# Optimization experiments

Measured on AMD Instinct MI355X. Metric: run time of the kernel, lower is better.

The kernel has to match this reference:

```python
import jax, jax.numpy as jnp
import numpy as np

D_MODEL = 256
D_HEAD = 64
N_HEAD = 8


def setup_inputs() -> dict:
    key = jax.random.key(0)
    ks = jax.random.split(key, 8)
    b, h, w = 32, 64, 64
    dk = D_HEAD * N_HEAD
    s = 1.0 / np.sqrt(D_MODEL)
    x = jax.random.normal(ks[0], (b, D_MODEL, h, w), dtype=jnp.float32)
    query = jax.random.normal(ks[1], (b, D_MODEL), dtype=jnp.float32)
    Wkv = jax.random.uniform(ks[2], (2 * dk, D_MODEL), jnp.float32, -s, s)
    bkv = jax.random.uniform(ks[3], (2 * dk,), jnp.float32, -s, s)
    Wq = jax.random.uniform(ks[4], (dk, D_MODEL), jnp.float32, -s, s)
    bq = jax.random.uniform(ks[5], (dk,), jnp.float32, -s, s)
    sf = 1.0 / np.sqrt(dk)
    Wfc = jax.random.uniform(ks[6], (D_MODEL, dk), jnp.float32, -sf, sf)
    bfc = jax.random.uniform(ks[7], (D_MODEL,), jnp.float32, -sf, sf)
    return {"x": x, "query": query, "Wkv": Wkv, "bkv": bkv, "Wq": Wq, "bq": bq, "Wfc": Wfc, "bfc": bfc}


def reference(x, query, Wkv, bkv, Wq, bq, Wfc, bfc):
    b, c, h, w = x.shape
    t = h * w
    scale = 1.0 / np.sqrt(D_HEAD).astype(np.float32)
    # 1x1 conv == per-pixel linear: (b, 2*n*d, t)
    kv = jnp.einsum('bchw,oc->bohw', x, Wkv).reshape(b, 2 * N_HEAD, D_HEAD, t)
    kv = kv + bkv.reshape(1, 2 * N_HEAD, D_HEAD, 1)
    k, v = kv[:, :N_HEAD], kv[:, N_HEAD:]  # each (b, n, d, t)
    q = (query @ Wq.T + bq).reshape(b, N_HEAD, D_HEAD)
    logits = jnp.einsum('bnd,bndj->bnj', q, k) * scale
    attn = jax.nn.softmax(logits, axis=2)
    out = jnp.einsum('bnj,bndj->bnd', attn, v).reshape(b, N_HEAD * D_HEAD)
    return jax.nn.relu(out @ Wfc.T + bfc)
```

## Files before the change

### kernel.cpp

```cpp
#include <hip/hip_runtime.h>
#include <hip/hip_bf16.h>

#define B_     32
#define C_     256
#define T_     4096
#define NH_    8
#define DH_    64

__global__ __launch_bounds__(256) void k_prep(
    const float* __restrict__ query, const float* __restrict__ Wkv,
    const float* __restrict__ bkv, const float* __restrict__ Wq,
    const float* __restrict__ bq, float* __restrict__ qWt,
    float* __restrict__ qb) {
  const int n = blockIdx.x;
  const int b = blockIdx.y;
  const int t = threadIdx.x;
  __shared__ float qrow_s[C_];
  __shared__ float psum[4 * 64];
  __shared__ float qsh[64];
  __shared__ float pb_s[64];

  qrow_s[t] = query[(size_t)b * C_ + t];
  __syncthreads();

  {
    const int d = t & 63, ch = t >> 6;
    const float* wrow = Wq + (size_t)(n * DH_ + d) * C_ + ch * 64;
    const float* qr = qrow_s + ch * 64;
    float s = 0.f;
    #pragma unroll
    for (int c = 0; c < 64; c += 4) {
      float4 w = *(const float4*)(wrow + c);
      s += w.x * qr[c] + w.y * qr[c + 1] + w.z * qr[c + 2] + w.w * qr[c + 3];
    }
    psum[ch * 64 + d] = s;
  }
  __syncthreads();
  if (t < 64)
    qsh[t] = bq[n * DH_ + t] + psum[t] + psum[64 + t] + psum[128 + t] + psum[192 + t];
  __syncthreads();

  const float scale = 0.125f;
  {
    const float* wk = Wkv + (size_t)(n * DH_) * C_ + t;
    float acc = 0.f;
    #pragma unroll 8
    for (int dd = 0; dd < DH_; ++dd) acc += qsh[dd] * wk[(size_t)dd * C_];
    qWt[((size_t)b * C_ + t) * NH_ + n] = acc * scale;
  }
  if (t < 64) pb_s[t] = qsh[t] * bkv[n * DH_ + t];
  __syncthreads();
  if (t == 0) {
    float s = 0.f;
    #pragma unroll 8
    for (int dd = 0; dd < 64; ++dd) s += pb_s[dd];
    qb[b * NH_ + n] = s * scale;
  }
}

__global__ __launch_bounds__(256, 4) void k_logits(
    const float* __restrict__ x, const float* __restrict__ qWt,
    const float* __restrict__ qbv, float* __restrict__ lgraw,
    float* __restrict__ stats) {
  const int jt = blockIdx.x;
  const int b  = blockIdx.y;
  const int t  = threadIdx.x;
  const int tj = t & 63;
  const int th = t >> 6;
  __shared__ float qws[C_ * NH_];
  __shared__ float red[4][64][17];

  {
    const float* src = qWt + (size_t)b * (C_ * NH_);
    *(float4*)&qws[t * 4] = *(const float4*)(src + t * 4);
    *(float4*)&qws[1024 + t * 4] = *(const float4*)(src + 1024 + t * 4);
  }
  __syncthreads();

  const int j = jt * 128 + tj * 2;
  const float* xb = x + ((size_t)b * C_ + th * 64) * T_ + j;

  float acc0[NH_], acc1[NH_];
  #pragma unroll
  for (int n = 0; n < NH_; ++n) {
    const float init = (th == 0) ? qbv[b * NH_ + n] : 0.f;
    acc0[n] = init; acc1[n] = init;
  }

  for (int c0 = 0; c0 < 64; c0 += 8) {
    float2 xv[8];
    #pragma unroll
    for (int cc = 0; cc < 8; ++cc)
      xv[cc] = *(const float2*)(xb + (size_t)(c0 + cc) * T_);
    #pragma unroll
    for (int cc = 0; cc < 8; ++cc) {
      const float4 w0 = *(const float4*)(qws + (th * 64 + c0 + cc) * 8);
      const float4 w1 = *(const float4*)(qws + (th * 64 + c0 + cc) * 8 + 4);
      acc0[0] += w0.x * xv[cc].x; acc1[0] += w0.x * xv[cc].y;
      acc0[1] += w0.y * xv[cc].x; acc1[1] += w0.y * xv[cc].y;
      acc0[2] += w0.z * xv[cc].x; acc1[2] += w0.z * xv[cc].y;
      acc0[3] += w0.w * xv[cc].x; acc1[3] += w0.w * xv[cc].y;
      acc0[4] += w1.x * xv[cc].x; acc1[4] += w1.x * xv[cc].y;
      acc0[5] += w1.y * xv[cc].x; acc1[5] += w1.y * xv[cc].y;
      acc0[6] += w1.z * xv[cc].x; acc1[6] += w1.z * xv[cc].y;
      acc0[7] += w1.w * xv[cc].x; acc1[7] += w1.w * xv[cc].y;
    }
  }

  if (th != 0) {
    float* r = &red[th][tj][0];
    #pragma unroll
    for (int n = 0; n < NH_; ++n) { r[n] = acc0[n]; r[8 + n] = acc1[n]; }
  }
  __syncthreads();
  if (th == 0) {
    #pragma unroll
    for (int q = 1; q < 4; ++q) {
      const float* r = &red[q][tj][0];
      #pragma unroll
      for (int n = 0; n < NH_; ++n) { acc0[n] += r[n]; acc1[n] += r[8 + n]; }
    }
    float* lg = lgraw + ((size_t)b * NH_) * T_ + j;
    #pragma unroll
    for (int n = 0; n < NH_; ++n) {
      float2 o; o.x = acc0[n]; o.y = acc1[n];
      *(float2*)(lg + (size_t)n * T_) = o;
    }
    float Mv[NH_], Sv[NH_];
    #pragma unroll
    for (int n = 0; n < NH_; ++n) {
      float mv = fmaxf(acc0[n], acc1[n]);
      #pragma unroll
      for (int o = 32; o >= 1; o >>= 1) mv = fmaxf(mv, __shfl_xor(mv, o));
      Mv[n] = mv;
    }
    #pragma unroll
    for (int n = 0; n < NH_; ++n) {
      float sv = expf(acc0[n] - Mv[n]) + expf(acc1[n] - Mv[n]);
      #pragma unroll
      for (int o = 32; o >= 1; o >>= 1) sv += __shfl_xor(sv, o);
      Sv[n] = sv;
    }
    if (tj == 0) {
      #pragma unroll
      for (int n = 0; n < NH_; ++n) {
        float2 o; o.x = Mv[n]; o.y = Sv[n];
        *(float2*)(stats + ((size_t)(b * NH_ + n) * 32 + jt) * 2) = o;
      }
    }
  }
}

#define BJ_  128
#define BJS_ 32
#define XPITCH_ 33
__global__ __launch_bounds__(256, 4) void k_xattn(
    const float* __restrict__ x, const float* __restrict__ lgraw,
    const float* __restrict__ stats, float* __restrict__ part) {
  const int jt = blockIdx.x;
  const int b  = blockIdx.y;
  const int j0 = jt * BJ_;
  const int t  = threadIdx.x;
  __shared__ float xs[C_ * XPITCH_];
  __shared__ float a_lds[NH_][BJS_];
  __shared__ float Msh[NH_];
  __shared__ float Sish[NH_];

  if (t < NH_) {
    const float* st = stats + (size_t)(b * NH_ + t) * 64;
    float M = -3.4e38f;
    #pragma unroll
    for (int k = 0; k < 32; ++k) M = fmaxf(M, st[k * 2]);
    float S = 0.f;
    #pragma unroll
    for (int k = 0; k < 32; ++k) S += st[k * 2 + 1] * expf(st[k * 2] - M);
    Msh[t] = M; Sish[t] = 1.0f / S;
  }

  const float* xb  = x + (size_t)b * C_ * T_;
  const float* lgb = lgraw + (size_t)b * NH_ * T_ + j0;

  float acc[NH_];
  #pragma unroll
  for (int n = 0; n < NH_; ++n) acc[n] = 0.f;

  const int cr = t >> 3;
  const int jc = (t & 7) * 4;
  const int an = t >> 5;
  const int aj = t & 31;

  for (int sIt = 0; sIt < BJ_ / BJS_; ++sIt) {
    const int js = sIt * BJS_;
    __syncthreads();
    #pragma unroll
    for (int p = 0; p < 8; ++p) {
      const int c = cr + p * 32;
      float4 vv = *(const float4*)(xb + (size_t)c * T_ + j0 + js + jc);
      float* dst = &xs[c * XPITCH_ + jc];
      dst[0] = vv.x; dst[1] = vv.y; dst[2] = vv.z; dst[3] = vv.w;
    }
    {
      const float lv = lgb[(size_t)an * T_ + js + aj];
      a_lds[an][aj] = expf(lv - Msh[an]) * Sish[an];
    }
    __syncthreads();
    const float* xr = &xs[t * XPITCH_];
    #pragma unroll 4
    for (int jj = 0; jj < BJS_; ++jj) {
      const float xv = xr[jj];
      #pragma unroll
      for (int n = 0; n < NH_; ++n)
        acc[n] += a_lds[n][jj] * xv;
    }
  }

  float* pb = part + ((size_t)b * 32 + jt) * (NH_ * C_);
  #pragma unroll
  for (int n = 0; n < NH_; ++n) pb[n * C_ + t] = acc[n];
}

__global__ __launch_bounds__(512) void k_tail(
    const float* __restrict__ part, const float* __restrict__ Wkv,
    const float* __restrict__ bkv, const float* __restrict__ Wfc,
    const float* __restrict__ bfc, float* __restrict__ out) {
  const int b = blockIdx.x;
  const int t = threadIdx.x;
  __shared__ float xa_s[NH_ * C_];
  __shared__ float ov_s[512];

  #pragma unroll
  for (int r = 0; r < 4; ++r) {
    const int idx = r * 512 + t;
    const float* pb = part + (size_t)b * 32 * (NH_ * C_) + idx;
    float s = 0.f;
    #pragma unroll
    for (int k = 0; k < 32; ++k) s += pb[(size_t)k * NH_ * C_];
    xa_s[idx] = s;
  }
  __syncthreads();

  {
    const int o = t;
    const float* wrow = Wkv + (size_t)(512 + o) * C_;
    const float* xa = &xa_s[(o >> 6) * C_];
    float s = bkv[512 + o];
    #pragma unroll 8
    for (int c = 0; c < C_; c += 4) {
      float4 w = *(const float4*)(wrow + c);
      s += w.x * xa[c] + w.y * xa[c + 1] + w.z * xa[c + 2] + w.w * xa[c + 3];
    }
    ov_s[o] = s;
  }
  __syncthreads();

  if (t < 256) {
    const float* wrow = Wfc + (size_t)t * 512;
    float s = bfc[t];
    #pragma unroll 8
    for (int o = 0; o < 512; o += 4) {
      float4 w = *(const float4*)(wrow + o);
      s += w.x * ov_s[o] + w.y * ov_s[o + 1] + w.z * ov_s[o + 2] + w.w * ov_s[o + 3];
    }
    out[(size_t)b * 256 + t] = fmaxf(s, 0.f);
  }
}

extern "C" void kernel_launch(void* const* d_in, const int* in_sizes, int n_in,
                              void* d_out, int out_size, void* d_ws, size_t ws_size,
                              hipStream_t stream) {
  const float* x     = (const float*)d_in[0];
  const float* query = (const float*)d_in[1];
  const float* Wkv   = (const float*)d_in[2];
  const float* bkv   = (const float*)d_in[3];
  const float* Wq    = (const float*)d_in[4];
  const float* bq    = (const float*)d_in[5];
  const float* Wfc   = (const float*)d_in[6];
  const float* bfc   = (const float*)d_in[7];
  float* out = (float*)d_out;
  float* ws  = (float*)d_ws;

  float* qWt   = ws;
  float* qb    = ws + 65536;
  float* stats = ws + 66048;
  float* lgraw = ws + 82432;
  float* part  = ws + 1131008;

  k_prep   <<<dim3(NH_, B_), 256, 0, stream>>>(query, Wkv, bkv, Wq, bq, qWt, qb);
  k_logits <<<dim3(32, B_),  256, 0, stream>>>(x, qWt, qb, lgraw, stats);
  k_xattn  <<<dim3(32, B_),  256, 0, stream>>>(x, lgraw, stats, part);
  k_tail   <<<B_,            512, 0, stream>>>(part, Wkv, bkv, Wfc, bfc, out);
}
```

Measured before the change: 273.5 us.

## Fuse logits and weighted-sum passes with local softmax, rescale partials in tail

Logits and the attention-weighted sum over x are merged into one kernel. Each block exponentiates against its own tile max, keeps the weights in LDS and reuses its x tile (now likely L2-hot) for the weighted sum. The raw-logits buffer round-trip and the second separate pass over x go away. Partials are rescaled by per-tile exp(m_k-M)/S in a new per-head tail kernel, and the final FC moves into its own kernel, which adds one launch but spreads the tail across more blocks.

After: 255.6 us. 1.07x faster.

```diff
diff --git a/kernel.cpp b/kernel.cpp
--- a/kernel.cpp
+++ b/kernel.cpp
@@ -58,21 +58,23 @@
   }
 }
 
-__global__ __launch_bounds__(256, 4) void k_logits(
+#define SCR_ 4352
+__global__ __launch_bounds__(256, 4) void k_fused(
     const float* __restrict__ x, const float* __restrict__ qWt,
-    const float* __restrict__ qbv, float* __restrict__ lgraw,
-    float* __restrict__ stats) {
+    const float* __restrict__ qbv, float* __restrict__ stats,
+    float* __restrict__ part) {
   const int jt = blockIdx.x;
   const int b  = blockIdx.y;
   const int t  = threadIdx.x;
   const int tj = t & 63;
   const int th = t >> 6;
   __shared__ float qws[C_ * NH_];
-  __shared__ float red[4][64][17];
+  __shared__ float scratch[SCR_];
+  __shared__ float a_w[NH_][128];
 
   {
     const float* src = qWt + (size_t)b * (C_ * NH_);
-    *(float4*)&qws[t * 4] = *(const float4*)(src + t * 4);
+    *(float4*)&qws[t * 4]        = *(const float4*)(src + t * 4);
     *(float4*)&qws[1024 + t * 4] = *(const float4*)(src + 1024 + t * 4);
   }
   __syncthreads();
@@ -108,7 +110,7 @@
   }
 
   if (th != 0) {
-    float* r = &red[th][tj][0];
+    float* r = &scratch[(th * 64 + tj) * 17];
     #pragma unroll
     for (int n = 0; n < NH_; ++n) { r[n] = acc0[n]; r[8 + n] = acc1[n]; }
   }
@@ -116,17 +118,11 @@
   if (th == 0) {
     #pragma unroll
     for (int q = 1; q < 4; ++q) {
-      const float* r = &red[q][tj][0];
+      const float* r = &scratch[(q * 64 + tj) * 17];
       #pragma unroll
       for (int n = 0; n < NH_; ++n) { acc0[n] += r[n]; acc1[n] += r[8 + n]; }
     }
-    float* lg = lgraw + ((size_t)b * NH_) * T_ + j;
-    #pragma unroll
-    for (int n = 0; n < NH_; ++n) {
-      float2 o; o.x = acc0[n]; o.y = acc1[n];
-      *(float2*)(lg + (size_t)n * T_) = o;
-    }
-    float Mv[NH_], Sv[NH_];
+    float Mv[NH_];
     #pragma unroll
     for (int n = 0; n < NH_; ++n) {
       float mv = fmaxf(acc0[n], acc1[n]);
@@ -134,9 +130,14 @@
       for (int o = 32; o >= 1; o >>= 1) mv = fmaxf(mv, __shfl_xor(mv, o));
       Mv[n] = mv;
     }
+    float Sv[NH_];
     #pragma unroll
     for (int n = 0; n < NH_; ++n) {
-      float sv = expf(acc0[n] - Mv[n]) + expf(acc1[n] - Mv[n]);
+      const float e0 = expf(acc0[n] - Mv[n]);
+      const float e1 = expf(acc1[n] - Mv[n]);
+      a_w[n][tj * 2]     = e0;
+      a_w[n][tj * 2 + 1] = e1;
+      float sv = e0 + e1;
       #pragma unroll
       for (int o = 32; o >= 1; o >>= 1) sv += __shfl_xor(sv, o);
       Sv[n] = sv;
@@ -149,68 +150,33 @@
       }
     }
   }
-}
-
-#define BJ_  128
-#define BJS_ 32
-#define XPITCH_ 33
-__global__ __launch_bounds__(256, 4) void k_xattn(
-    const float* __restrict__ x, const float* __restrict__ lgraw,
-    const float* __restrict__ stats, float* __restrict__ part) {
-  const int jt = blockIdx.x;
-  const int b  = blockIdx.y;
-  const int j0 = jt * BJ_;
-  const int t  = threadIdx.x;
-  __shared__ float xs[C_ * XPITCH_];
-  __shared__ float a_lds[NH_][BJS_];
-  __shared__ float Msh[NH_];
-  __shared__ float Sish[NH_];
-
-  if (t < NH_) {
-    const float* st = stats + (size_t)(b * NH_ + t) * 64;
-    float M = -3.4e38f;
-    #pragma unroll
-    for (int k = 0; k < 32; ++k) M = fmaxf(M, st[k * 2]);
-    float S = 0.f;
-    #pragma unroll
-    for (int k = 0; k < 32; ++k) S += st[k * 2 + 1] * expf(st[k * 2] - M);
-    Msh[t] = M; Sish[t] = 1.0f / S;
-  }
-
-  const float* xb  = x + (size_t)b * C_ * T_;
-  const float* lgb = lgraw + (size_t)b * NH_ * T_ + j0;
-
+
+  const float* xb2 = x + (size_t)b * C_ * T_ + jt * 128;
+  const int cr = t >> 2;
+  const int jc = (t & 3) * 4;
   float acc[NH_];
   #pragma unroll
   for (int n = 0; n < NH_; ++n) acc[n] = 0.f;
 
-  const int cr = t >> 3;
-  const int jc = (t & 7) * 4;
-  const int an = t >> 5;
-  const int aj = t & 31;
-
-  for (int sIt = 0; sIt < BJ_ / BJS_; ++sIt) {
-    const int js = sIt * BJS_;
+  for (int sIt = 0; sIt < 8; ++sIt) {
+    const int js = sIt * 16;
     __syncthreads();
     #pragma unroll
-    for (int p = 0; p < 8; ++p) {
-      const int c = cr + p * 32;
-      float4 vv = *(const float4*)(xb + (size_t)c * T_ + j0 + js + jc);
-      float* dst = &xs[c * XPITCH_ + jc];
+    for (int p = 0; p < 4; ++p) {
+      const int c = cr + p * 64;
+      float4 vv = *(const float4*)(xb2 + (size_t)c * T_ + js + jc);
+      float* dst = &scratch[c * 17 + jc];
       dst[0] = vv.x; dst[1] = vv.y; dst[2] = vv.z; dst[3] = vv.w;
     }
-    {
-      const float lv = lgb[(size_t)an * T_ + js + aj];
-      a_lds[an][aj] = expf(lv - Msh[an]) * Sish[an];
-    }
     __syncthreads();
-    const float* xr = &xs[t * XPITCH_];
-    #pragma unroll 4
-    for (int jj = 0; jj < BJS_; ++jj) {
+    const float* xr = &scratch[t * 17];
+    #pragma unroll
+    for (int jj = 0; jj < 16; ++jj) {
       const float xv = xr[jj];
+      const int jg = js + jj;
       #pragma unroll
       for (int n = 0; n < NH_; ++n)
-        acc[n] += a_lds[n][jj] * xv;
+        acc[n] += a_w[n][jg] * xv;
     }
   }
 
@@ -219,50 +185,76 @@
   for (int n = 0; n < NH_; ++n) pb[n * C_ + t] = acc[n];
 }
 
-__global__ __launch_bounds__(512) void k_tail(
-    const float* __restrict__ part, const float* __restrict__ Wkv,
-    const float* __restrict__ bkv, const float* __restrict__ Wfc,
+__global__ __launch_bounds__(256) void k_out2(
+    const float* __restrict__ part, const float* __restrict__ stats,
+    const float* __restrict__ Wkv, const float* __restrict__ bkv,
+    float* __restrict__ outvG) {
+  const int n = blockIdx.x;
+  const int b = blockIdx.y;
+  const int t = threadIdx.x;
+  __shared__ float sc[32];
+  __shared__ float xa[C_];
+  __shared__ float psum[4][64];
+
+  if (t < 32) {
+    const float* st = stats + (size_t)(b * NH_ + n) * 64;
+    const float mk = st[2 * t], sk = st[2 * t + 1];
+    float M = mk;
+    #pragma unroll
+    for (int o = 16; o >= 1; o >>= 1) M = fmaxf(M, __shfl_xor(M, o));
+    const float e = expf(mk - M);
+    float S = sk * e;
+    #pragma unroll
+    for (int o = 16; o >= 1; o >>= 1) S += __shfl_xor(S, o);
+    sc[t] = e / S;
+  }
+  __syncthreads();
+
+  {
+    const float* pb = part + (size_t)b * 32 * (NH_ * C_) + n * C_ + t;
+    float s = 0.f;
+    #pragma unroll
+    for (int k = 0; k < 32; ++k) s += sc[k] * pb[(size_t)k * (NH_ * C_)];
+    xa[t] = s;
+  }
+  __syncthreads();
+
+  {
+    const int d = t & 63, q = t >> 6;
+    const float* wrow = Wkv + (size_t)(512 + n * 64 + d) * C_ + q * 64;
+    const float* xq = xa + q * 64;
+    float s = 0.f;
+    #pragma unroll
+    for (int c = 0; c < 64; c += 4) {
+      float4 w = *(const float4*)(wrow + c);
+      s += w.x * xq[c] + w.y * xq[c + 1] + w.z * xq[c + 2] + w.w * xq[c + 3];
+    }
+    psum[q][d] = s;
+  }
+  __syncthreads();
+  if (t < 64)
+    outvG[(size_t)b * 512 + n * 64 + t] =
+        bkv[512 + n * 64 + t] + psum[0][t] + psum[1][t] + psum[2][t] + psum[3][t];
+}
+
+__global__ __launch_bounds__(256) void k_fc(
+    const float* __restrict__ outvG, const float* __restrict__ Wfc,
     const float* __restrict__ bfc, float* __restrict__ out) {
+  __shared__ float ov[512];
   const int b = blockIdx.x;
   const int t = threadIdx.x;
-  __shared__ float xa_s[NH_ * C_];
-  __shared__ float ov_s[512];
-
-  #pragma unroll
-  for (int r = 0; r < 4; ++r) {
-    const int idx = r * 512 + t;
-    const float* pb = part + (size_t)b * 32 * (NH_ * C_) + idx;
-    float s = 0.f;
-    #pragma unroll
-    for (int k = 0; k < 32; ++k) s += pb[(size_t)k * NH_ * C_];
-    xa_s[idx] = s;
-  }
-  __syncthreads();
-
-  {
-    const int o = t;
-    const float* wrow = Wkv + (size_t)(512 + o) * C_;
-    const float* xa = &xa_s[(o >> 6) * C_];
-    float s = bkv[512 + o];
-    #pragma unroll 8
-    for (int c = 0; c < C_; c += 4) {
-      float4 w = *(const float4*)(wrow + c);
-      s += w.x * xa[c] + w.y * xa[c + 1] + w.z * xa[c + 2] + w.w * xa[c + 3];
-    }
-    ov_s[o] = s;
-  }
-  __syncthreads();
-
-  if (t < 256) {
-    const float* wrow = Wfc + (size_t)t * 512;
-    float s = bfc[t];
-    #pragma unroll 8
-    for (int o = 0; o < 512; o += 4) {
-      float4 w = *(const float4*)(wrow + o);
-      s += w.x * ov_s[o] + w.y * ov_s[o + 1] + w.z * ov_s[o + 2] + w.w * ov_s[o + 3];
-    }
-    out[(size_t)b * 256 + t] = fmaxf(s, 0.f);
-  }
+  ov[t] = outvG[(size_t)b * 512 + t];
+  ov[256 + t] = outvG[(size_t)b * 512 + 256 + t];
+  __syncthreads();
+
+  const float* wrow = Wfc + (size_t)t * 512;
+  float s = bfc[t];
+  #pragma unroll 8
+  for (int o = 0; o < 512; o += 4) {
+    float4 w = *(const float4*)(wrow + o);
+    s += w.x * ov[o] + w.y * ov[o + 1] + w.z * ov[o + 2] + w.w * ov[o + 3];
+  }
+  out[(size_t)b * 256 + t] = fmaxf(s, 0.f);
 }
 
 extern "C" void kernel_launch(void* const* d_in, const int* in_sizes, int n_in,
@@ -282,11 +274,11 @@
   float* qWt   = ws;
   float* qb    = ws + 65536;
   float* stats = ws + 66048;
-  float* lgraw = ws + 82432;
-  float* part  = ws + 1131008;
-
-  k_prep   <<<dim3(NH_, B_), 256, 0, stream>>>(query, Wkv, bkv, Wq, bq, qWt, qb);
-  k_logits <<<dim3(32, B_),  256, 0, stream>>>(x, qWt, qb, lgraw, stats);
-  k_xattn  <<<dim3(32, B_),  256, 0, stream>>>(x, lgraw, stats, part);
-  k_tail   <<<B_,            512, 0, stream>>>(part, Wkv, bkv, Wfc, bfc, out);
-}
+  float* part  = ws + 82432;
+  float* outvG = ws + 2179584;
+
+  k_prep  <<<dim3(NH_, B_), 256, 0, stream>>>(query, Wkv, bkv, Wq, bq, qWt, qb);
+  k_fused <<<dim3(32, B_),  256, 0, stream>>>(x, qWt, qb, stats, part);
+  k_out2  <<<dim3(NH_, B_), 256, 0, stream>>>(part, stats, Wkv, bkv, outvG);
+  k_fc    <<<B_,            256, 0, stream>>>(outvG, Wfc, bfc, out);
+}
```
